# Kernel tuning notes

Measured on AMD Instinct MI355X. Metric: run time of the kernel, lower is better.

## Reference

```python
import jax, jax.numpy as jnp
import numpy as np

TAU = 2.0
V_TH = 0.5
SG_ALPHA = 4.0
BN_EPS = 1e-5
NUM_HEADS = 8

@jax.custom_vjp
def spike_fn(x):
    return (x >= 0.0).astype(x.dtype)

def _spike_fwd(x):
    return (x >= 0.0).astype(x.dtype), x

def _spike_bwd(x, g):
    s = jax.nn.sigmoid(SG_ALPHA * x)
    return (g * SG_ALPHA * s * (1.0 - s),)

spike_fn.defvjp(_spike_fwd, _spike_bwd)

def lif(x_seq):
    """Multi-step LIF (spikingjelly step_mode='m'): x_seq [T, ...] -> spikes [T, ...].
    v <- v + (x - v)/tau ; spike = H(v - v_th) ; hard reset with detached spike."""
    def step(v, x):
        v = v + (x - v) / TAU
        s = spike_fn(v - V_TH)
        v = v * (1.0 - jax.lax.stop_gradient(s))
        return v, s
    _, s_seq = jax.lax.scan(step, jnp.zeros_like(x_seq[0]), x_seq)
    return s_seq

def conv1x1(x, w, b=None):
    # x: [T,B,C,H,W], w: [Cout,Cin]
    y = jnp.einsum('tbchw,oc->tbohw', x, w)
    if b is not None:
        y = y + b[:, None, None]
    return y

def bn(x, p):
    # eval-mode BatchNorm2d; p = [gamma, beta, mean, var] each [C]
    g, b, m, v = p[0], p[1], p[2], p[3]
    scale = g / jnp.sqrt(v + BN_EPS)
    return x * scale[:, None, None] + (b - m * scale)[:, None, None]

def setup_inputs() -> dict:
    key = jax.random.key(0)
    ks = jax.random.split(key, 20)
    T, B, C, H, W = 4, 8, 512, 32, 32
    Ch = 2048
    def bn_params(k, c):
        kk = jax.random.split(k, 4)
        gamma = jax.random.uniform(kk[0], (c,), jnp.float32, 0.5, 1.5)
        beta = jax.random.normal(kk[1], (c,), jnp.float32) * 0.1
        mean = jax.random.normal(kk[2], (c,), jnp.float32) * 0.1
        var = jax.random.uniform(kk[3], (c,), jnp.float32, 0.5, 1.5)
        return jnp.stack([gamma, beta, mean, var])
    s = 1.0 / np.sqrt(C)
    sh = 1.0 / np.sqrt(Ch)
    return {
        'x': jax.random.normal(ks[0], (T, B, C, H, W), jnp.float32),
        'q_w': jax.random.normal(ks[1], (C, C), jnp.float32) * s,
        'q_bn': bn_params(ks[2], C),
        'k_w': jax.random.normal(ks[3], (C, C), jnp.float32) * s,
        'k_bn': bn_params(ks[4], C),
        'v_w': jax.random.normal(ks[5], (C, C), jnp.float32) * s,
        'v_bn': bn_params(ks[6], C),
        'th_w': jax.random.normal(ks[7], (NUM_HEADS, NUM_HEADS), jnp.float32) / np.sqrt(NUM_HEADS),
        'proj_w': jax.random.normal(ks[8], (C, C), jnp.float32) * s,
        'proj_b': jax.random.normal(ks[9], (C,), jnp.float32) * 0.02,
        'proj_bn': bn_params(ks[10], C),
        'fc1_w': jax.random.normal(ks[11], (Ch, C), jnp.float32) * s,
        'fc1_b': jax.random.normal(ks[12], (Ch,), jnp.float32) * 0.02,
        'fc1_bn': bn_params(ks[13], Ch),
        'fc2_w': jax.random.normal(ks[14], (C, Ch), jnp.float32) * sh,
        'fc2_b': jax.random.normal(ks[15], (C,), jnp.float32) * 0.02,
        'fc2_bn': bn_params(ks[16], C),
    }

def reference(x, q_w, q_bn, k_w, k_bn, v_w, v_bn, th_w, proj_w, proj_b, proj_bn,
              fc1_w, fc1_b, fc1_bn, fc2_w, fc2_b, fc2_bn):
    T, B, C, H, W = x.shape
    N = H * W
    h = NUM_HEADS
    d = C // h

    # ---- MS_SSA_Conv ----
    identity = x
    xs = lif(x)  # shortcut_lif

    def to_heads(t):  # [T,B,C,H,W] -> [T,B,h,N,d]
        t = t.reshape(T, B, C, N).transpose(0, 1, 3, 2)        # [T,B,N,C]
        return t.reshape(T, B, N, h, d).transpose(0, 1, 3, 2, 4)

    q = to_heads(lif(bn(conv1x1(xs, q_w), q_bn)))
    k = to_heads(lif(bn(conv1x1(xs, k_w), k_bn)))
    v = to_heads(lif(bn(conv1x1(xs, v_w), v_bn)))

    kv = (k * v).sum(axis=3, keepdims=True)                    # [T,B,h,1,d]
    kv = jnp.einsum('tbhod,gh->tbgod', kv, th_w)               # talking heads (Conv1d k=1)
    kv = lif(kv)                                               # talking_heads_lif

    x_att = q * kv                                             # [T,B,h,N,d]
    x_att = x_att.transpose(0, 1, 2, 4, 3).reshape(T, B, C, H, W)
    x_out = bn(conv1x1(x_att, proj_w, proj_b), proj_bn) + identity

    # ---- MS_MLP_Conv (res=False since hidden != in) ----
    identity2 = x_out
    hdn = lif(bn(conv1x1(x_out, fc1_w, fc1_b), fc1_bn))
    out = lif(bn(conv1x1(hdn, fc2_w, fc2_b), fc2_bn)) + identity2
    return out
```

## Files before the change

kernel.cpp:

```cpp
#include <hip/hip_runtime.h>
#include <hip/hip_bf16.h>
#include <type_traits>

#define T_STEPS 4
#define B_SZ 8
#define C_IN 512
#define CH 2048
#define N_SP 1024
#define NHEADS 8
#define HDIM 64
#define S_C ((size_t)B_SZ * C_IN * N_SP)

typedef unsigned char u8;

__global__ __launch_bounds__(256) void lif_x_kernel(const float* __restrict__ in,
                                                    u8* __restrict__ out)
{
    size_t i = (size_t)blockIdx.x * 256 + threadIdx.x;
    float v = 0.0f;
    #pragma unroll
    for (int t = 0; t < T_STEPS; ++t) {
        float x = in[(size_t)t * S_C + i];
        v += (x - v) * 0.5f;
        u8 s = (v >= 0.5f) ? 1 : 0;
        out[(size_t)t * S_C + i] = s;
        v = s ? 0.0f : v;
    }
}

template<int MODE, bool BIAS, typename InT>
__global__ __launch_bounds__(256) void gemm_fused(
    const InT* __restrict__ X,
    const float* __restrict__ W,
    const float* __restrict__ bnp,
    const float* __restrict__ bias,
    const float* __restrict__ kvs,
    const float* res,
    void* Yv,
    int K, int Co)
{
    const int N = N_SP;
    const int b = blockIdx.z;
    const int coBase = blockIdx.y * 64;
    const int nBase = blockIdx.x * 64;
    const int tid = threadIdx.x;
    const int tx = tid & 15, ty = tid >> 4;

    __shared__ float As[16][68];
    __shared__ float Bs[16][68];

    const int arow = tid >> 2, ak0 = (tid & 3) * 4;
    const int brow = tid >> 4, bn0 = (tid & 15) * 4;

    float scale[4], shift[4];
    #pragma unroll
    for (int i = 0; i < 4; ++i) {
        const int co = coBase + ty * 4 + i;
        const float g  = bnp[co];
        const float be = bnp[Co + co];
        const float mn = bnp[2 * Co + co];
        const float vr = bnp[3 * Co + co];
        scale[i] = g / sqrtf(vr + 1e-5f);
        shift[i] = be - mn * scale[i];
        if (BIAS) shift[i] += bias[co] * scale[i];
    }

    float vst[4][4] = {};

    for (int t = 0; t < T_STEPS; ++t) {
        const size_t tb = (size_t)(t * B_SZ + b);
        const InT* Xb = X + tb * (size_t)K * N;
        float acc[4][4] = {};

        for (int k0 = 0; k0 < K; k0 += 16) {
            float4 av = *reinterpret_cast<const float4*>(
                W + (size_t)(coBase + arow) * K + k0 + ak0);
            As[ak0 + 0][arow] = av.x;
            As[ak0 + 1][arow] = av.y;
            As[ak0 + 2][arow] = av.z;
            As[ak0 + 3][arow] = av.w;

            float4 bv;
            if constexpr (std::is_same<InT, u8>::value) {
                uchar4 u = *reinterpret_cast<const uchar4*>(
                    Xb + (size_t)(k0 + brow) * N + nBase + bn0);
                bv = make_float4((float)u.x, (float)u.y, (float)u.z, (float)u.w);
            } else {
                bv = *reinterpret_cast<const float4*>(
                    Xb + (size_t)(k0 + brow) * N + nBase + bn0);
            }
            if constexpr (MODE == 1) {
                float m = kvs[tb * K + k0 + brow];
                bv.x *= m; bv.y *= m; bv.z *= m; bv.w *= m;
            }
            *reinterpret_cast<float4*>(&Bs[brow][bn0]) = bv;

            __syncthreads();
            #pragma unroll
            for (int kk = 0; kk < 16; ++kk) {
                float4 a = *reinterpret_cast<const float4*>(&As[kk][ty * 4]);
                float4 bq = *reinterpret_cast<const float4*>(&Bs[kk][tx * 4]);
                float aa[4] = {a.x, a.y, a.z, a.w};
                float bb[4] = {bq.x, bq.y, bq.z, bq.w};
                #pragma unroll
                for (int i = 0; i < 4; ++i)
                    #pragma unroll
                    for (int j = 0; j < 4; ++j)
                        acc[i][j] += aa[i] * bb[j];
            }
            __syncthreads();
        }

        #pragma unroll
        for (int i = 0; i < 4; ++i) {
            const int co = coBase + ty * 4 + i;
            const size_t rowOff = (tb * Co + co) * (size_t)N + nBase + tx * 4;
            if constexpr (MODE == 0) {
                u8 sj[4];
                #pragma unroll
                for (int j = 0; j < 4; ++j) {
                    const float y = acc[i][j] * scale[i] + shift[i];
                    float v = vst[i][j];
                    v += (y - v) * 0.5f;
                    const u8 s = (v >= 0.5f) ? 1 : 0;
                    sj[j] = s;
                    vst[i][j] = s ? 0.0f : v;
                }
                *reinterpret_cast<uchar4*>((u8*)Yv + rowOff) =
                    make_uchar4(sj[0], sj[1], sj[2], sj[3]);
            } else if constexpr (MODE == 1) {
                const float4 r = *reinterpret_cast<const float4*>(res + rowOff);
                float4 o;
                o.x = acc[i][0] * scale[i] + shift[i] + r.x;
                o.y = acc[i][1] * scale[i] + shift[i] + r.y;
                o.z = acc[i][2] * scale[i] + shift[i] + r.z;
                o.w = acc[i][3] * scale[i] + shift[i] + r.w;
                *reinterpret_cast<float4*>((float*)Yv + rowOff) = o;
            } else {
                const float4 r = *reinterpret_cast<const float4*>(res + rowOff);
                float o[4] = {r.x, r.y, r.z, r.w};
                #pragma unroll
                for (int j = 0; j < 4; ++j) {
                    const float y = acc[i][j] * scale[i] + shift[i];
                    float v = vst[i][j];
                    v += (y - v) * 0.5f;
                    const u8 s = (v >= 0.5f) ? 1 : 0;
                    o[j] += s ? 1.0f : 0.0f;
                    vst[i][j] = s ? 0.0f : v;
                }
                *reinterpret_cast<float4*>((float*)Yv + rowOff) =
                    make_float4(o[0], o[1], o[2], o[3]);
            }
        }
    }
}

__global__ __launch_bounds__(256) void kv_reduce(const u8* __restrict__ ks,
                                                 const u8* __restrict__ vs,
                                                 float* __restrict__ kv)
{
    const int row = blockIdx.x * 4 + (threadIdx.x >> 6);
    const int lane = threadIdx.x & 63;
    const u8* kp = ks + (size_t)row * N_SP;
    const u8* vp = vs + (size_t)row * N_SP;
    int acc = 0;
    #pragma unroll
    for (int n = 0; n < N_SP; n += 256) {
        uchar4 a = *reinterpret_cast<const uchar4*>(kp + n + lane * 4);
        uchar4 c = *reinterpret_cast<const uchar4*>(vp + n + lane * 4);
        acc += (a.x & c.x) + (a.y & c.y) + (a.z & c.z) + (a.w & c.w);
    }
    #pragma unroll
    for (int off = 32; off; off >>= 1) acc += __shfl_down(acc, off, 64);
    if (lane == 0) kv[row] = (float)acc;
}

__global__ __launch_bounds__(256) void th_lif(const float* __restrict__ kvraw,
                                              const float* __restrict__ th,
                                              float* __restrict__ kvs)
{
    const int i = blockIdx.x * 256 + threadIdx.x;
    const int b = i >> 9;
    const int c = i & 511;
    const int g = c >> 6;
    const int dd = c & 63;
    float v = 0.0f;
    #pragma unroll
    for (int t = 0; t < T_STEPS; ++t) {
        const float* base = kvraw + ((size_t)t * B_SZ + b) * C_IN;
        float x = 0.0f;
        #pragma unroll
        for (int hh = 0; hh < NHEADS; ++hh)
            x += base[hh * HDIM + dd] * th[g * NHEADS + hh];
        v += (x - v) * 0.5f;
        const float s = (v >= 0.5f) ? 1.0f : 0.0f;
        kvs[((size_t)t * B_SZ + b) * C_IN + c] = s;
        v = (s != 0.0f) ? 0.0f : v;
    }
}

extern "C" void kernel_launch(void* const* d_in, const int* in_sizes, int n_in,
                              void* d_out, int out_size, void* d_ws, size_t ws_size,
                              hipStream_t stream)
{
    const float* x       = (const float*)d_in[0];
    const float* q_w     = (const float*)d_in[1];
    const float* q_bn    = (const float*)d_in[2];
    const float* k_w     = (const float*)d_in[3];
    const float* k_bn    = (const float*)d_in[4];
    const float* v_w     = (const float*)d_in[5];
    const float* v_bn    = (const float*)d_in[6];
    const float* th_w    = (const float*)d_in[7];
    const float* proj_w  = (const float*)d_in[8];
    const float* proj_b  = (const float*)d_in[9];
    const float* proj_bn = (const float*)d_in[10];
    const float* fc1_w   = (const float*)d_in[11];
    const float* fc1_b   = (const float*)d_in[12];
    const float* fc1_bn  = (const float*)d_in[13];
    const float* fc2_w   = (const float*)d_in[14];
    const float* fc2_b   = (const float*)d_in[15];
    const float* fc2_bn  = (const float*)d_in[16];
    float* out = (float*)d_out;

    const size_t SLOT = (size_t)T_STEPS * S_C;
    u8* sp  = (u8*)d_ws;
    u8* xs  = sp;
    u8* qs  = sp + SLOT;
    u8* ks  = sp + 2 * SLOT;
    u8* vs  = sp + 3 * SLOT;
    u8* hdn = sp;
    float* kvraw = (float*)(sp + 4 * SLOT);
    float* kvs   = kvraw + (size_t)T_STEPS * B_SZ * C_IN;

    lif_x_kernel<<<(int)(S_C / 256), 256, 0, stream>>>(x, xs);

    dim3 gC(16, 8, 8);
    gemm_fused<0, false, u8><<<gC, 256, 0, stream>>>(xs, q_w, q_bn, nullptr, nullptr, nullptr, qs, C_IN, C_IN);
    gemm_fused<0, false, u8><<<gC, 256, 0, stream>>>(xs, k_w, k_bn, nullptr, nullptr, nullptr, ks, C_IN, C_IN);
    gemm_fused<0, false, u8><<<gC, 256, 0, stream>>>(xs, v_w, v_bn, nullptr, nullptr, nullptr, vs, C_IN, C_IN);

    kv_reduce<<<(T_STEPS * B_SZ * C_IN) / 4, 256, 0, stream>>>(ks, vs, kvraw);

    th_lif<<<(B_SZ * C_IN) / 256, 256, 0, stream>>>(kvraw, th_w, kvs);

    gemm_fused<1, true, u8><<<gC, 256, 0, stream>>>(qs, proj_w, proj_bn, proj_b, kvs, x, out, C_IN, C_IN);

    dim3 gCh(16, 32, 8);
    gemm_fused<0, true, float><<<gCh, 256, 0, stream>>>(out, fc1_w, fc1_bn, fc1_b, nullptr, nullptr, hdn, C_IN, CH);

    gemm_fused<2, true, u8><<<gC, 256, 0, stream>>>(hdn, fc2_w, fc2_bn, fc2_b, nullptr, out, out, CH, C_IN);
}
```

Measured before the change: 2.946 ms.

## Fuse Q/K/V GEMMs into one launch and load activations directly to registers

Replaces the tiled GEMM with one that stages only weights in shared memory (32x64 tile) and streams spike or float activations from global memory straight into registers, widening the per-thread tile to 4x8 over a 128-wide spatial block. The three Q/K/V projections become a single launch that picks weights, BN params and outputs by blockIdx.y. K and Co are now compile-time template constants. The aim is fewer launches, less shared-memory traffic and more FMAs per load, at the cost of uncoalesced-style per-thread global loads and higher register pressure.

```diff
diff --git a/kernel.cpp b/kernel.cpp
--- a/kernel.cpp
+++ b/kernel.cpp
@@ -1,17 +1,14 @@
 #include <hip/hip_runtime.h>
-#include <hip/hip_bf16.h>
-#include <type_traits>
+
+typedef unsigned char u8;
+typedef unsigned int u32;
 
 #define T_STEPS 4
 #define B_SZ 8
 #define C_IN 512
 #define CH 2048
 #define N_SP 1024
-#define NHEADS 8
-#define HDIM 64
 #define S_C ((size_t)B_SZ * C_IN * N_SP)
-
-typedef unsigned char u8;
 
 __global__ __launch_bounds__(256) void lif_x_kernel(const float* __restrict__ in,
                                                     u8* __restrict__ out)
@@ -28,128 +25,182 @@
     }
 }
 
-template<int MODE, bool BIAS, typename InT>
-__global__ __launch_bounds__(256) void gemm_fused(
-    const InT* __restrict__ X,
-    const float* __restrict__ W,
-    const float* __restrict__ bnp,
+template<int MODE, int BSRC, bool BIAS, int K, int CO, bool F3>
+__global__ __launch_bounds__(256) void mm(
+    const float* __restrict__ W0, const float* __restrict__ W1, const float* __restrict__ W2,
+    const void* __restrict__ Xv,
+    const float* __restrict__ bn0, const float* __restrict__ bn1, const float* __restrict__ bn2,
     const float* __restrict__ bias,
-    const float* __restrict__ kvs,
-    const float* res,
-    void* Yv,
-    int K, int Co)
-{
-    const int N = N_SP;
+    const float* __restrict__ kvsf,
+    const float* __restrict__ res,
+    void* Y0, void* Y1, void* Y2)
+{
+    __shared__ float Ws[32][64];
     const int b = blockIdx.z;
-    const int coBase = blockIdx.y * 64;
-    const int nBase = blockIdx.x * 64;
+    int sel = 0, cb = blockIdx.y;
+    if (F3) { sel = blockIdx.y >> 3; cb = blockIdx.y & 7; }
+    const float* W   = (!F3 || sel == 0) ? W0  : (sel == 1 ? W1  : W2);
+    const float* bnp = (!F3 || sel == 0) ? bn0 : (sel == 1 ? bn1 : bn2);
+    void* Yv         = (!F3 || sel == 0) ? Y0  : (sel == 1 ? Y1  : Y2);
+
+    const int coBase = cb * 64;
+    const int nBase = blockIdx.x * 128;
     const int tid = threadIdx.x;
     const int tx = tid & 15, ty = tid >> 4;
-
-    __shared__ float As[16][68];
-    __shared__ float Bs[16][68];
-
-    const int arow = tid >> 2, ak0 = (tid & 3) * 4;
-    const int brow = tid >> 4, bn0 = (tid & 15) * 4;
+    const int n0 = nBase + tx * 8;
+    const int wco = tid & 63, wk = (tid >> 6) * 8;
 
     float scale[4], shift[4];
     #pragma unroll
     for (int i = 0; i < 4; ++i) {
         const int co = coBase + ty * 4 + i;
-        const float g  = bnp[co];
-        const float be = bnp[Co + co];
-        const float mn = bnp[2 * Co + co];
-        const float vr = bnp[3 * Co + co];
+        const float g = bnp[co], be = bnp[CO + co];
+        const float mn = bnp[2 * CO + co], vr = bnp[3 * CO + co];
         scale[i] = g / sqrtf(vr + 1e-5f);
         shift[i] = be - mn * scale[i];
         if (BIAS) shift[i] += bias[co] * scale[i];
     }
 
-    float vst[4][4] = {};
+    float vst[4][8];
+    if (MODE != 1) {
+        #pragma unroll
+        for (int i = 0; i < 4; ++i)
+            #pragma unroll
+            for (int j = 0; j < 8; ++j) vst[i][j] = 0.0f;
+    }
 
     for (int t = 0; t < T_STEPS; ++t) {
-        const size_t tb = (size_t)(t * B_SZ + b);
-        const InT* Xb = X + tb * (size_t)K * N;
-        float acc[4][4] = {};
-
-        for (int k0 = 0; k0 < K; k0 += 16) {
-            float4 av = *reinterpret_cast<const float4*>(
-                W + (size_t)(coBase + arow) * K + k0 + ak0);
-            As[ak0 + 0][arow] = av.x;
-            As[ak0 + 1][arow] = av.y;
-            As[ak0 + 2][arow] = av.z;
-            As[ak0 + 3][arow] = av.w;
-
-            float4 bv;
-            if constexpr (std::is_same<InT, u8>::value) {
-                uchar4 u = *reinterpret_cast<const uchar4*>(
-                    Xb + (size_t)(k0 + brow) * N + nBase + bn0);
-                bv = make_float4((float)u.x, (float)u.y, (float)u.z, (float)u.w);
-            } else {
-                bv = *reinterpret_cast<const float4*>(
-                    Xb + (size_t)(k0 + brow) * N + nBase + bn0);
-            }
-            if constexpr (MODE == 1) {
-                float m = kvs[tb * K + k0 + brow];
-                bv.x *= m; bv.y *= m; bv.z *= m; bv.w *= m;
-            }
-            *reinterpret_cast<float4*>(&Bs[brow][bn0]) = bv;
-
+        const int tb = t * B_SZ + b;
+        const u8* Xu = (const u8*)Xv + (size_t)tb * K * N_SP;
+        const float* Xf = (const float*)Xv + (size_t)tb * K * N_SP;
+        float acc[4][8];
+        #pragma unroll
+        for (int i = 0; i < 4; ++i)
+            #pragma unroll
+            for (int j = 0; j < 8; ++j) acc[i][j] = 0.0f;
+
+        for (int k0 = 0; k0 < K; k0 += 32) {
             __syncthreads();
-            #pragma unroll
-            for (int kk = 0; kk < 16; ++kk) {
-                float4 a = *reinterpret_cast<const float4*>(&As[kk][ty * 4]);
-                float4 bq = *reinterpret_cast<const float4*>(&Bs[kk][tx * 4]);
-                float aa[4] = {a.x, a.y, a.z, a.w};
-                float bb[4] = {bq.x, bq.y, bq.z, bq.w};
-                #pragma unroll
-                for (int i = 0; i < 4; ++i)
-                    #pragma unroll
-                    for (int j = 0; j < 4; ++j)
-                        acc[i][j] += aa[i] * bb[j];
+            {
+                const float* wp = W + (size_t)(coBase + wco) * K + k0 + wk;
+                float4 w0 = *reinterpret_cast<const float4*>(wp);
+                float4 w1 = *reinterpret_cast<const float4*>(wp + 4);
+                Ws[wk + 0][wco] = w0.x; Ws[wk + 1][wco] = w0.y;
+                Ws[wk + 2][wco] = w0.z; Ws[wk + 3][wco] = w0.w;
+                Ws[wk + 4][wco] = w1.x; Ws[wk + 5][wco] = w1.y;
+                Ws[wk + 6][wco] = w1.z; Ws[wk + 7][wco] = w1.w;
             }
             __syncthreads();
+
+            if (BSRC <= 1) {
+                #pragma unroll
+                for (int h = 0; h < 2; ++h) {
+                    uint2 xu[16];
+                    #pragma unroll
+                    for (int q = 0; q < 16; ++q)
+                        xu[q] = *reinterpret_cast<const uint2*>(
+                            Xu + (size_t)(k0 + h * 16 + q) * N_SP + n0);
+                    #pragma unroll
+                    for (int q = 0; q < 16; ++q) {
+                        const int kk = h * 16 + q;
+                        float4 wf = *reinterpret_cast<const float4*>(&Ws[kk][ty * 4]);
+                        float wa[4] = {wf.x, wf.y, wf.z, wf.w};
+                        float xf[8];
+                        xf[0] = (float)( xu[q].x        & 0xFFu);
+                        xf[1] = (float)((xu[q].x >> 8 ) & 0xFFu);
+                        xf[2] = (float)((xu[q].x >> 16) & 0xFFu);
+                        xf[3] = (float)( xu[q].x >> 24        );
+                        xf[4] = (float)( xu[q].y        & 0xFFu);
+                        xf[5] = (float)((xu[q].y >> 8 ) & 0xFFu);
+                        xf[6] = (float)((xu[q].y >> 16) & 0xFFu);
+                        xf[7] = (float)( xu[q].y >> 24        );
+                        if (BSRC == 1) {
+                            const float m = kvsf[(size_t)tb * K + k0 + kk];
+                            #pragma unroll
+                            for (int j = 0; j < 8; ++j) xf[j] *= m;
+                        }
+                        #pragma unroll
+                        for (int i = 0; i < 4; ++i)
+                            #pragma unroll
+                            for (int j = 0; j < 8; ++j)
+                                acc[i][j] += wa[i] * xf[j];
+                    }
+                }
+            } else {
+                #pragma unroll
+                for (int h = 0; h < 8; ++h) {
+                    float4 xa[4][2];
+                    #pragma unroll
+                    for (int q = 0; q < 4; ++q) {
+                        const float* xp = Xf + (size_t)(k0 + h * 4 + q) * N_SP + n0;
+                        xa[q][0] = *reinterpret_cast<const float4*>(xp);
+                        xa[q][1] = *reinterpret_cast<const float4*>(xp + 4);
+                    }
+                    #pragma unroll
+                    for (int q = 0; q < 4; ++q) {
+                        const int kk = h * 4 + q;
+                        float4 wf = *reinterpret_cast<const float4*>(&Ws[kk][ty * 4]);
+                        float wa[4] = {wf.x, wf.y, wf.z, wf.w};
+                        float xf[8] = {xa[q][0].x, xa[q][0].y, xa[q][0].z, xa[q][0].w,
+                                       xa[q][1].x, xa[q][1].y, xa[q][1].z, xa[q][1].w};
+                        #pragma unroll
+                        for (int i = 0; i < 4; ++i)
+                            #pragma unroll
+                            for (int j = 0; j < 8; ++j)
+                                acc[i][j] += wa[i] * xf[j];
+                    }
+                }
+            }
         }
 
         #pragma unroll
         for (int i = 0; i < 4; ++i) {
             const int co = coBase + ty * 4 + i;
-            const size_t rowOff = (tb * Co + co) * (size_t)N + nBase + tx * 4;
-            if constexpr (MODE == 0) {
-                u8 sj[4];
-                #pragma unroll
-                for (int j = 0; j < 4; ++j) {
+            const size_t rowoff = ((size_t)tb * CO + co) * N_SP + n0;
+            if (MODE == 0) {
+                u32 p0 = 0, p1 = 0;
+                #pragma unroll
+                for (int j = 0; j < 8; ++j) {
                     const float y = acc[i][j] * scale[i] + shift[i];
                     float v = vst[i][j];
                     v += (y - v) * 0.5f;
-                    const u8 s = (v >= 0.5f) ? 1 : 0;
-                    sj[j] = s;
+                    const u32 s = (v >= 0.5f) ? 1u : 0u;
                     vst[i][j] = s ? 0.0f : v;
+                    if (j < 4) p0 |= s << (8 * j); else p1 |= s << (8 * (j - 4));
                 }
-                *reinterpret_cast<uchar4*>((u8*)Yv + rowOff) =
-                    make_uchar4(sj[0], sj[1], sj[2], sj[3]);
-            } else if constexpr (MODE == 1) {
-                const float4 r = *reinterpret_cast<const float4*>(res + rowOff);
-                float4 o;
-                o.x = acc[i][0] * scale[i] + shift[i] + r.x;
-                o.y = acc[i][1] * scale[i] + shift[i] + r.y;
-                o.z = acc[i][2] * scale[i] + shift[i] + r.z;
-                o.w = acc[i][3] * scale[i] + shift[i] + r.w;
-                *reinterpret_cast<float4*>((float*)Yv + rowOff) = o;
+                uint2 pk; pk.x = p0; pk.y = p1;
+                *reinterpret_cast<uint2*>((u8*)Yv + rowoff) = pk;
+            } else if (MODE == 1) {
+                float4 r0 = *reinterpret_cast<const float4*>(res + rowoff);
+                float4 r1 = *reinterpret_cast<const float4*>(res + rowoff + 4);
+                float rr[8] = {r0.x, r0.y, r0.z, r0.w, r1.x, r1.y, r1.z, r1.w};
+                float o[8];
+                #pragma unroll
+                for (int j = 0; j < 8; ++j)
+                    o[j] = acc[i][j] * scale[i] + shift[i] + rr[j];
+                float4 s0 = {o[0], o[1], o[2], o[3]};
+                float4 s1 = {o[4], o[5], o[6], o[7]};
+                *reinterpret_cast<float4*>((float*)Yv + rowoff) = s0;
+                *reinterpret_cast<float4*>((float*)Yv + rowoff + 4) = s1;
             } else {
-                const float4 r = *reinterpret_cast<const float4*>(res + rowOff);
-                float o[4] = {r.x, r.y, r.z, r.w};
-                #pragma unroll
-                for (int j = 0; j < 4; ++j) {
+                float* op = (float*)Yv + rowoff;
+                float4 r0 = *reinterpret_cast<const float4*>(op);
+                float4 r1 = *reinterpret_cast<const float4*>(op + 4);
+                float rr[8] = {r0.x, r0.y, r0.z, r0.w, r1.x, r1.y, r1.z, r1.w};
+                float o[8];
+                #pragma unroll
+                for (int j = 0; j < 8; ++j) {
                     const float y = acc[i][j] * scale[i] + shift[i];
                     float v = vst[i][j];
                     v += (y - v) * 0.5f;
-                    const u8 s = (v >= 0.5f) ? 1 : 0;
-                    o[j] += s ? 1.0f : 0.0f;
+                    const u32 s = (v >= 0.5f) ? 1u : 0u;
                     vst[i][j] = s ? 0.0f : v;
+                    o[j] = rr[j] + (s ? 1.0f : 0.0f);
                 }
-                *reinterpret_cast<float4*>((float*)Yv + rowOff) =
-                    make_float4(o[0], o[1], o[2], o[3]);
+                float4 s0 = {o[0], o[1], o[2], o[3]};
+                float4 s1 = {o[4], o[5], o[6], o[7]};
+                *reinterpret_cast<float4*>(op) = s0;
+                *reinterpret_cast<float4*>(op + 4) = s1;
             }
         }
     }
@@ -190,8 +241,8 @@
         const float* base = kvraw + ((size_t)t * B_SZ + b) * C_IN;
         float x = 0.0f;
         #pragma unroll
-        for (int hh = 0; hh < NHEADS; ++hh)
-            x += base[hh * HDIM + dd] * th[g * NHEADS + hh];
+        for (int hh = 0; hh < 8; ++hh)
+            x += base[hh * 64 + dd] * th[g * 8 + hh];
         v += (x - v) * 0.5f;
         const float s = (v >= 0.5f) ? 1.0f : 0.0f;
         kvs[((size_t)t * B_SZ + b) * C_IN + c] = s;
@@ -222,31 +273,33 @@
     const float* fc2_bn  = (const float*)d_in[16];
     float* out = (float*)d_out;
 
+    u8* ws = (u8*)d_ws;
     const size_t SLOT = (size_t)T_STEPS * S_C;
-    u8* sp  = (u8*)d_ws;
-    u8* xs  = sp;
-    u8* qs  = sp + SLOT;
-    u8* ks  = sp + 2 * SLOT;
-    u8* vs  = sp + 3 * SLOT;
-    u8* hdn = sp;
-    float* kvraw = (float*)(sp + 4 * SLOT);
-    float* kvs   = kvraw + (size_t)T_STEPS * B_SZ * C_IN;
+    u8* xs = ws;
+    u8* qs = ws + SLOT;
+    u8* ks = ws + 2 * SLOT;
+    u8* vs = ws + 3 * SLOT;
+    float* kvraw = (float*)(ws + 4 * SLOT);
+    float* kvsf  = kvraw + (size_t)T_STEPS * B_SZ * C_IN;
+    u8* hdn = ws;
 
     lif_x_kernel<<<(int)(S_C / 256), 256, 0, stream>>>(x, xs);
 
-    dim3 gC(16, 8, 8);
-    gemm_fused<0, false, u8><<<gC, 256, 0, stream>>>(xs, q_w, q_bn, nullptr, nullptr, nullptr, qs, C_IN, C_IN);
-    gemm_fused<0, false, u8><<<gC, 256, 0, stream>>>(xs, k_w, k_bn, nullptr, nullptr, nullptr, ks, C_IN, C_IN);
-    gemm_fused<0, false, u8><<<gC, 256, 0, stream>>>(xs, v_w, v_bn, nullptr, nullptr, nullptr, vs, C_IN, C_IN);
+    mm<0, 0, false, 512, 512, true><<<dim3(8, 24, 8), 256, 0, stream>>>(
+        q_w, k_w, v_w, xs, q_bn, k_bn, v_bn, nullptr, nullptr, nullptr, qs, ks, vs);
 
     kv_reduce<<<(T_STEPS * B_SZ * C_IN) / 4, 256, 0, stream>>>(ks, vs, kvraw);
-
-    th_lif<<<(B_SZ * C_IN) / 256, 256, 0, stream>>>(kvraw, th_w, kvs);
-
-    gemm_fused<1, true, u8><<<gC, 256, 0, stream>>>(qs, proj_w, proj_bn, proj_b, kvs, x, out, C_IN, C_IN);
-
-    dim3 gCh(16, 32, 8);
-    gemm_fused<0, true, float><<<gCh, 256, 0, stream>>>(out, fc1_w, fc1_bn, fc1_b, nullptr, nullptr, hdn, C_IN, CH);
-
-    gemm_fused<2, true, u8><<<gC, 256, 0, stream>>>(hdn, fc2_w, fc2_bn, fc2_b, nullptr, out, out, CH, C_IN);
-}
+    th_lif<<<(B_SZ * C_IN) / 256, 256, 0, stream>>>(kvraw, th_w, kvsf);
+
+    mm<1, 1, true, 512, 512, false><<<dim3(8, 8, 8), 256, 0, stream>>>(
+        proj_w, nullptr, nullptr, qs, proj_bn, nullptr, nullptr, proj_b, kvsf, x,
+        out, nullptr, nullptr);
+
+    mm<0, 2, true, 512, 2048, false><<<dim3(8, 32, 8), 256, 0, stream>>>(
+        fc1_w, nullptr, nullptr, out, fc1_bn, nullptr, nullptr, fc1_b, nullptr, nullptr,
+        hdn, nullptr, nullptr);
+
+    mm<2, 0, true, 2048, 512, false><<<dim3(8, 8, 8), 256, 0, stream>>>(
+        fc2_w, nullptr, nullptr, hdn, fc2_bn, nullptr, nullptr, fc2_b, nullptr, nullptr,
+        out, nullptr, nullptr);
+}
```

Result: slower. 3.495 ms (+18.6%).
